# Performance work log

Measured on AMD Instinct MI355X. Metric: run time of the kernel, lower is better.

Reference implementation:

```python
import jax, jax.numpy as jnp
import numpy as np

B, L, DIN = 32, 512, 768
H, DH = 16, 48
DOUT = H * DH
NEG = 1e12


def setup_inputs() -> dict:
    key = jax.random.key(0)
    ks = jax.random.split(key, 8)
    lim = float(np.sqrt(6.0 / (DIN + DOUT)))  # xavier_uniform
    return {
        "Q_seq": jax.random.normal(ks[0], (B, L, DIN), jnp.float32),
        "K_seq": jax.random.normal(ks[1], (B, L, DIN), jnp.float32),
        "V_seq": jax.random.normal(ks[2], (B, L, DIN), jnp.float32),
        "WQ": jax.random.uniform(ks[3], (DIN, DOUT), jnp.float32, -lim, lim),
        "WK": jax.random.uniform(ks[4], (DIN, DOUT), jnp.float32, -lim, lim),
        "WV": jax.random.uniform(ks[5], (DIN, DOUT), jnp.float32, -lim, lim),
        "Q_len": jax.random.randint(ks[6], (B, 1), 0, L, jnp.int64),
        "V_len": jax.random.randint(ks[7], (B, 1), 0, L, jnp.int64),
    }


def reference(Q_seq, K_seq, V_seq, WQ, WK, WV, Q_len, V_len):
    b, l = Q_seq.shape[0], Q_seq.shape[1]
    # projections -> [B, H, L, DH]
    q = (Q_seq @ WQ).reshape(b, l, H, DH).transpose(0, 2, 1, 3)
    k = (K_seq @ WK).reshape(b, l, H, DH).transpose(0, 2, 1, 3)
    v = (V_seq @ WV).reshape(b, l, H, DH).transpose(0, 2, 1, 3)
    # scaled scores [B, H, Lq, Lk]
    A = jnp.einsum("bhqd,bhkd->bhqk", q, k) / jnp.sqrt(jnp.float32(DH))
    # key-length additive mask (original: scatter+cumsum == arange < len)
    mask_k = (jnp.arange(l) < V_len[:, 0][:, None]).astype(A.dtype)  # [B, Lk]
    A = A - (1.0 - mask_k)[:, None, None, :] * NEG
    # causal mask (mask_right=True): subtract on strictly upper triangle
    A = A - jnp.triu(jnp.ones((l, l), A.dtype), 1) * NEG
    A = jax.nn.softmax(A, axis=-1)
    # original quirk: O = A^T @ V  -> O[b,h,k,d] = sum_q A[b,h,q,k] V[b,h,q,d]
    O = jnp.einsum("bhqk,bhqd->bkhd", A, v).reshape(b, l, DOUT)
    # query-length multiplicative mask on output
    mask_q = (jnp.arange(l) < Q_len[:, 0][:, None]).astype(O.dtype)  # [B, L]
    return O * mask_q[:, :, None]
```

## Files before the change

kernel.cpp:

```cpp
#include <hip/hip_runtime.h>
#include <stdint.h>

#define B_    32
#define L_    512
#define DIN_  768
#define H_    16
#define DH_   48
#define DOUT_ 768
#define NHEADS (B_ * H_)
#define HEADELEMS (L_ * DH_)
#define MROWS (B_ * L_)

typedef short bf16x8 __attribute__((ext_vector_type(8)));
typedef float f32x4  __attribute__((ext_vector_type(4)));

__device__ __forceinline__ uint16_t f2bf(float f) {
  uint32_t u = __float_as_uint(f);
  u += 0x7fffu + ((u >> 16) & 1u);
  return (uint16_t)(u >> 16);
}
__device__ __forceinline__ uint32_t pack2bf(float lo, float hi) {
  uint32_t a = __float_as_uint(lo);
  a += 0x7fffu + ((a >> 16) & 1u);
  uint32_t b = __float_as_uint(hi);
  b += 0x7fffu + ((b >> 16) & 1u);
  return (a >> 16) | (b & 0xffff0000u);
}
__device__ __forceinline__ void gload_lds16(const void* g, void* l) {
  __builtin_amdgcn_global_load_lds(
      (const __attribute__((address_space(1))) uint32_t*)g,
      (__attribute__((address_space(3))) uint32_t*)l, 16, 0, 0);
}
__device__ __forceinline__ bf16x8 lds_frag8(const uint16_t* p) {
  union { uint2 u[2]; bf16x8 v; } x;
  x.u[0] = *(const uint2*)(p);
  x.u[1] = *(const uint2*)(p + 4);
  return x.v;
}

__global__ void lens_kernel(const int* __restrict__ qlen_raw,
                            const int* __restrict__ vlen_raw,
                            int* __restrict__ lens) {
  __shared__ int is64[2];
  int t = threadIdx.x;
  if (t < 2) {
    const int* src = (t == 0) ? qlen_raw : vlen_raw;
    int o = 0;
    for (int i = 0; i < 16; ++i) o |= src[2 * i + 1];
    is64[t] = (o == 0) ? 1 : 0;
  }
  __syncthreads();
  int which = t >> 5;
  int i = t & 31;
  const int* src = which ? vlen_raw : qlen_raw;
  lens[t] = is64[which] ? src[2 * i] : src[i];
}

__global__ void wconv_kernel(const float* __restrict__ WQ,
                             const float* __restrict__ WK,
                             const float* __restrict__ WV,
                             uint16_t* __restrict__ Wt) {
  const int z = blockIdx.z;
  const float* W = (z == 0) ? WQ : (z == 1) ? WK : WV;
  const float sc = (z == 0) ? 0.14433756729740643f : 1.0f;
  uint16_t* dst = Wt + (size_t)z * DIN_ * DOUT_;
  const int n  = blockIdx.x * 256 + threadIdx.x;
  const int k4 = blockIdx.y * 4;
  float f0 = W[(size_t)(k4 + 0) * DOUT_ + n] * sc;
  float f1 = W[(size_t)(k4 + 1) * DOUT_ + n] * sc;
  float f2 = W[(size_t)(k4 + 2) * DOUT_ + n] * sc;
  float f3 = W[(size_t)(k4 + 3) * DOUT_ + n] * sc;
  uint2 p;
  p.x = pack2bf(f0, f1);
  p.y = pack2bf(f2, f3);
  *(uint2*)&dst[(size_t)n * DIN_ + k4] = p;
}

__global__ __launch_bounds__(512, 4) void mfma_proj(
    const float* __restrict__ Xq, const float* __restrict__ Xk,
    const float* __restrict__ Xv, const uint16_t* __restrict__ Wt,
    uint16_t* __restrict__ qh, uint16_t* __restrict__ kh,
    uint16_t* __restrict__ vh) {
  const int z = blockIdx.z;
  const float* X = (z == 0) ? Xq : (z == 1) ? Xk : Xv;
  uint16_t* dst  = (z == 0) ? qh : (z == 1) ? kh : vh;
  const uint16_t* W = Wt + (size_t)z * DIN_ * DOUT_;

  __shared__ uint16_t As[2][128][32];
  __shared__ uint16_t Bs[2][256][32];

  const int t  = threadIdx.x;
  const int m0 = blockIdx.x * 128;
  const int n0 = blockIdx.y * 256;

  const int csw = (t & 3) ^ ((t >> 3) & 3);

  const float* aptr = X + (size_t)(m0 + (t >> 2)) * DIN_ + csw * 8;
  char* aWb = (char*)&As[0][0][0] + (t >> 2) * 64 + (t & 3) * 16;

  const uint16_t* bptr0 = W + (size_t)(n0 + (t >> 2)) * DIN_ + csw * 8;
  const uint16_t* bptr1 = W + (size_t)(n0 + 128 + (t >> 2)) * DIN_ + csw * 8;
  char* bB = (char*)&Bs[0][0][0] + t * 16;

  const int w = t >> 6, lane = t & 63;
  const int wm = (w & 1) * 64, wn = (w >> 1) * 64;
  const int fr = lane & 15;
  const int quad = lane >> 4;

  f32x4 acc[4][4];
#pragma unroll
  for (int i = 0; i < 4; ++i)
#pragma unroll
    for (int j = 0; j < 4; ++j) acc[i][j] = f32x4{0.f, 0.f, 0.f, 0.f};

  {
    gload_lds16(bptr0, bB);
    gload_lds16(bptr1, bB + 8192);
    float4 x0 = *(const float4*)(aptr);
    float4 x1 = *(const float4*)(aptr + 4);
    uint4 pA;
    pA.x = pack2bf(x0.x, x0.y); pA.y = pack2bf(x0.z, x0.w);
    pA.z = pack2bf(x1.x, x1.y); pA.w = pack2bf(x1.z, x1.w);
    *(uint4*)aWb = pA;
    __syncthreads();
  }

  int cur = 0;
  for (int kt = 0; kt < DIN_ / 32; ++kt) {
    const int nxt = cur ^ 1;
    float4 x0{}, x1{};
    const bool pre = (kt + 1 < DIN_ / 32);
    if (pre) {
      const int k0 = (kt + 1) * 32;
      gload_lds16(bptr0 + k0, bB + nxt * 16384);
      gload_lds16(bptr1 + k0, bB + nxt * 16384 + 8192);
      x0 = *(const float4*)(aptr + k0);
      x1 = *(const float4*)(aptr + k0 + 4);
    }

    bf16x8 af[4], bfr[4];
#pragma unroll
    for (int i = 0; i < 4; ++i) {
      const int r = wm + i * 16 + fr;
      af[i]  = *(const bf16x8*)&As[cur][r][(quad ^ ((r >> 1) & 3)) * 8];
    }
#pragma unroll
    for (int j = 0; j < 4; ++j) {
      const int r = wn + j * 16 + fr;
      bfr[j] = *(const bf16x8*)&Bs[cur][r][(quad ^ ((r >> 1) & 3)) * 8];
    }
#pragma unroll
    for (int mt = 0; mt < 4; ++mt)
#pragma unroll
      for (int nt = 0; nt < 4; ++nt)
        acc[mt][nt] = __builtin_amdgcn_mfma_f32_16x16x32_bf16(
            af[mt], bfr[nt], acc[mt][nt], 0, 0, 0);

    if (pre) {
      uint4 pA;
      pA.x = pack2bf(x0.x, x0.y); pA.y = pack2bf(x0.z, x0.w);
      pA.z = pack2bf(x1.x, x1.y); pA.w = pack2bf(x1.z, x1.w);
      *(uint4*)(aWb + nxt * 8192) = pA;
    }
    __syncthreads();
    cur = nxt;
  }

#pragma unroll
  for (int mt = 0; mt < 4; ++mt) {
#pragma unroll
    for (int r = 0; r < 4; ++r) {
      const int m  = m0 + wm + mt * 16 + quad * 4 + r;
      const int bb = m >> 9;
      const int l  = m & 511;
#pragma unroll
      for (int nt = 0; nt < 4; ++nt) {
        const int n = n0 + wn + nt * 16 + fr;
        const int h = n / DH_;
        const int d = n - h * DH_;
        dst[(((size_t)bb * H_ + h) * L_ + l) * DH_ + d] = f2bf(acc[mt][nt][r]);
      }
    }
  }
}

__global__ __launch_bounds__(256, 2) void attn_mfma(
    const uint16_t* __restrict__ qh, const uint16_t* __restrict__ kh,
    const uint16_t* __restrict__ vh, const int* __restrict__ lens,
    float* __restrict__ out) {
  const int bh = blockIdx.x;
  const int b  = bh >> 4;
  const int h  = bh & 15;
  const int t    = threadIdx.x;
  const int w    = t >> 6;
  const int lane = t & 63;
  const int l15  = lane & 15;
  const int quad = lane >> 4;

  const int qlen = lens[b];
  const int vlen = lens[32 + b];
  const bool deg = (vlen == 0);
  const size_t head = (size_t)bh * HEADELEMS;

  __shared__ uint16_t Pt[4][128][36];
  __shared__ uint16_t Vt[48][36];
  __shared__ float    prt[4][32];

  const uint16_t* qbase = qh + head;
  const uint16_t* kbase = kh + head;
  const uint16_t* vbase = vh + head;

  f32x4 Oacc[8][3];
#pragma unroll
  for (int i = 0; i < 8; ++i)
#pragma unroll
    for (int dt = 0; dt < 3; ++dt) Oacc[i][dt] = f32x4{0.f, 0.f, 0.f, 0.f};

  for (int g = 0; g < 16; ++g) {
    const int q0 = g * 32;
    const int lim = q0 + 31 - 16 * w;

    __syncthreads();

    if (t < 192) {
      const int vq = t & 31, oct = t >> 5;
      uint4 u = *(const uint4*)(vbase + (size_t)(q0 + vq) * DH_ + oct * 8);
      const int d0 = oct * 8;
      Vt[d0 + 0][vq] = (uint16_t)(u.x);
      Vt[d0 + 1][vq] = (uint16_t)(u.x >> 16);
      Vt[d0 + 2][vq] = (uint16_t)(u.y);
      Vt[d0 + 3][vq] = (uint16_t)(u.y >> 16);
      Vt[d0 + 4][vq] = (uint16_t)(u.z);
      Vt[d0 + 5][vq] = (uint16_t)(u.z >> 16);
      Vt[d0 + 6][vq] = (uint16_t)(u.w);
      Vt[d0 + 7][vq] = (uint16_t)(u.w >> 16);
    }

    bf16x8 aq[2][2];
#pragma unroll
    for (int mt = 0; mt < 2; ++mt) {
      const uint16_t* qp = qbase + (size_t)(q0 + mt * 16 + l15) * DH_;
      aq[mt][0] = *(const bf16x8*)(qp + quad * 8);
      bf16x8 zz = {0, 0, 0, 0, 0, 0, 0, 0};
      aq[mt][1] = zz;
      if (quad < 2) aq[mt][1] = *(const bf16x8*)(qp + 32 + quad * 8);
    }

    float lrun[2][4];
#pragma unroll
    for (int mt = 0; mt < 2; ++mt)
#pragma unroll
      for (int r = 0; r < 4; ++r) lrun[mt][r] = 0.0f;

#pragma unroll
    for (int i = 0; i < 8; ++i) {
      if (64 * i > lim) continue;
      const int kb = 64 * i + 16 * w;
      f32x4 s0 = {0.f, 0.f, 0.f, 0.f};
      f32x4 s1 = {0.f, 0.f, 0.f, 0.f};
      if (!deg) {
        const uint16_t* kp = kbase + (size_t)(kb + l15) * DH_;
        bf16x8 bk0 = *(const bf16x8*)(kp + quad * 8);
        bf16x8 bk1 = {0, 0, 0, 0, 0, 0, 0, 0};
        if (quad < 2) bk1 = *(const bf16x8*)(kp + 32 + quad * 8);
        s0 = __builtin_amdgcn_mfma_f32_16x16x32_bf16(aq[0][0], bk0, s0, 0, 0, 0);
        s0 = __builtin_amdgcn_mfma_f32_16x16x32_bf16(aq[0][1], bk1, s0, 0, 0, 0);
        s1 = __builtin_amdgcn_mfma_f32_16x16x32_bf16(aq[1][0], bk0, s1, 0, 0, 0);
        s1 = __builtin_amdgcn_mfma_f32_16x16x32_bf16(aq[1][1], bk1, s1, 0, 0, 0);
      }
      const int kc  = kb + l15;
      const int row = i * 16 + l15;
#pragma unroll
      for (int mt = 0; mt < 2; ++mt) {
        f32x4 sv = (mt == 0) ? s0 : s1;
        float p4[4];
#pragma unroll
        for (int r = 0; r < 4; ++r) {
          const int qrow = q0 + mt * 16 + quad * 4 + r;
          float e;
          if (deg) {
            e = (kc <= qrow) ? 1.0f : 0.0f;
          } else {
            e = (kc < vlen && kc <= qrow) ? __expf(sv[r]) : 0.0f;
          }
          lrun[mt][r] += e;
          p4[r] = e;
        }
        const int col = mt * 16 + quad * 4;
        *(uint32_t*)&Pt[w][row][col]     = pack2bf(p4[0], p4[1]);
        *(uint32_t*)&Pt[w][row][col + 2] = pack2bf(p4[2], p4[3]);
      }
    }

#pragma unroll
    for (int mt = 0; mt < 2; ++mt)
#pragma unroll
      for (int r = 0; r < 4; ++r) {
        float l = lrun[mt][r];
#pragma unroll
        for (int off = 1; off < 16; off <<= 1) l += __shfl_xor(l, off, 64);
        lrun[mt][r] = l;
      }
    if (l15 == 0) {
#pragma unroll
      for (int mt = 0; mt < 2; ++mt)
#pragma unroll
        for (int r = 0; r < 4; ++r)
          prt[w][mt * 16 + quad * 4 + r] = lrun[mt][r];
    }
    __syncthreads();

    {
      const int q = t & 31;
      const float inv = __builtin_amdgcn_rcpf(
          prt[0][q] + prt[1][q] + prt[2][q] + prt[3][q]);
#pragma unroll
      for (int j = 0; j < 6; ++j) {
        const int d = (t >> 5) + 8 * j;
        float f = __uint_as_float((uint32_t)Vt[d][q] << 16) * inv;
        Vt[d][q] = f2bf(f);
      }
    }
    __syncthreads();

    bf16x8 bv[3];
#pragma unroll
    for (int dt = 0; dt < 3; ++dt)
      bv[dt] = lds_frag8(&Vt[dt * 16 + l15][quad * 8]);
#pragma unroll
    for (int i = 0; i < 8; ++i) {
      if (64 * i > lim) continue;
      bf16x8 ap = lds_frag8(&Pt[w][i * 16 + l15][quad * 8]);
#pragma unroll
      for (int dt = 0; dt < 3; ++dt)
        Oacc[i][dt] = __builtin_amdgcn_mfma_f32_16x16x32_bf16(
            ap, bv[dt], Oacc[i][dt], 0, 0, 0);
    }
  }

#pragma unroll
  for (int i = 0; i < 8; ++i) {
#pragma unroll
    for (int r = 0; r < 4; ++r) {
      const int k_abs = 64 * i + 16 * w + quad * 4 + r;
      const float msk = (k_abs < qlen) ? 1.0f : 0.0f;
      float* orow = out + (size_t)(b * L_ + k_abs) * DOUT_ + h * DH_;
#pragma unroll
      for (int dt = 0; dt < 3; ++dt)
        orow[dt * 16 + l15] = Oacc[i][dt][r] * msk;
    }
  }
}

extern "C" void kernel_launch(void* const* d_in, const int* in_sizes, int n_in,
                              void* d_out, int out_size, void* d_ws, size_t ws_size,
                              hipStream_t stream) {
  const float* Qs  = (const float*)d_in[0];
  const float* Kse = (const float*)d_in[1];
  const float* Vs  = (const float*)d_in[2];
  const float* WQ  = (const float*)d_in[3];
  const float* WK  = (const float*)d_in[4];
  const float* WV  = (const float*)d_in[5];
  const int*   Qlen = (const int*)d_in[6];
  const int*   Vlen = (const int*)d_in[7];
  float* out = (float*)d_out;

  char* ws = (char*)d_ws;
  int* lens = (int*)ws;
  uint16_t* qh  = (uint16_t*)(ws + 256);
  uint16_t* kh  = qh + (size_t)B_ * H_ * L_ * DH_;
  uint16_t* vh  = kh + (size_t)B_ * H_ * L_ * DH_;
  uint16_t* Wt  = vh + (size_t)B_ * H_ * L_ * DH_;

  lens_kernel<<<1, 64, 0, stream>>>(Qlen, Vlen, lens);
  wconv_kernel<<<dim3(3, 192, 3), 256, 0, stream>>>(WQ, WK, WV, Wt);
  mfma_proj<<<dim3(MROWS / 128, DOUT_ / 256, 3), 512, 0, stream>>>(
      Qs, Kse, Vs, Wt, qh, kh, vh);
  attn_mfma<<<NHEADS, 256, 0, stream>>>(qh, kh, vh, lens, out);
}
```

Before: 331.7 us.

## Triple-buffer weight tiles in projection GEMM with explicit vmcnt waits

After: 335.4 us. No clear change (+1.1%).

```diff
diff --git a/kernel.cpp b/kernel.cpp
--- a/kernel.cpp
+++ b/kernel.cpp
@@ -87,11 +87,12 @@
   const uint16_t* W = Wt + (size_t)z * DIN_ * DOUT_;
 
   __shared__ uint16_t As[2][128][32];
-  __shared__ uint16_t Bs[2][256][32];
+  __shared__ uint16_t Bs[3][256][32];
 
   const int t  = threadIdx.x;
   const int m0 = blockIdx.x * 128;
   const int n0 = blockIdx.y * 256;
+  const int NKT = DIN_ / 32;
 
   const int csw = (t & 3) ^ ((t >> 3) & 3);
 
@@ -113,41 +114,47 @@
 #pragma unroll
     for (int j = 0; j < 4; ++j) acc[i][j] = f32x4{0.f, 0.f, 0.f, 0.f};
 
-  {
-    gload_lds16(bptr0, bB);
-    gload_lds16(bptr1, bB + 8192);
-    float4 x0 = *(const float4*)(aptr);
-    float4 x1 = *(const float4*)(aptr + 4);
-    uint4 pA;
-    pA.x = pack2bf(x0.x, x0.y); pA.y = pack2bf(x0.z, x0.w);
-    pA.z = pack2bf(x1.x, x1.y); pA.w = pack2bf(x1.z, x1.w);
-    *(uint4*)aWb = pA;
-    __syncthreads();
-  }
-
-  int cur = 0;
-  for (int kt = 0; kt < DIN_ / 32; ++kt) {
-    const int nxt = cur ^ 1;
-    float4 x0{}, x1{};
-    const bool pre = (kt + 1 < DIN_ / 32);
-    if (pre) {
-      const int k0 = (kt + 1) * 32;
-      gload_lds16(bptr0 + k0, bB + nxt * 16384);
-      gload_lds16(bptr1 + k0, bB + nxt * 16384 + 8192);
-      x0 = *(const float4*)(aptr + k0);
-      x1 = *(const float4*)(aptr + k0 + 4);
-    }
+  float4 x0, x1;
+
+#define STAGE_(j_)                                          \
+  {                                                         \
+    const int k0_ = (j_) * 32;                              \
+    x0 = *(const float4*)(aptr + k0_);                      \
+    x1 = *(const float4*)(aptr + k0_ + 4);                  \
+    gload_lds16(bptr0 + k0_, bB + ((j_) % 3) * 16384);      \
+    gload_lds16(bptr1 + k0_, bB + ((j_) % 3) * 16384 + 8192); \
+  }
+#define PACKA_(j_)                                          \
+  {                                                         \
+    uint4 pA_;                                              \
+    pA_.x = pack2bf(x0.x, x0.y); pA_.y = pack2bf(x0.z, x0.w); \
+    pA_.z = pack2bf(x1.x, x1.y); pA_.w = pack2bf(x1.z, x1.w); \
+    *(uint4*)(aWb + ((j_) % 2) * 8192) = pA_;               \
+  }
+
+  STAGE_(0);
+  PACKA_(0);
+  STAGE_(1);
+  asm volatile("s_waitcnt vmcnt(4) lgkmcnt(0)" ::: "memory");
+  __builtin_amdgcn_s_barrier();
+  __builtin_amdgcn_sched_barrier(0);
+
+  for (int kt = 0; kt < NKT; ++kt) {
+    if (kt + 1 < NKT) PACKA_(kt + 1);
+    if (kt + 2 < NKT) STAGE_(kt + 2);
 
     bf16x8 af[4], bfr[4];
+    const uint16_t(*Acur)[32] = As[kt & 1];
+    const uint16_t(*Bcur)[32] = Bs[kt % 3];
 #pragma unroll
     for (int i = 0; i < 4; ++i) {
       const int r = wm + i * 16 + fr;
-      af[i]  = *(const bf16x8*)&As[cur][r][(quad ^ ((r >> 1) & 3)) * 8];
+      af[i]  = *(const bf16x8*)&Acur[r][(quad ^ ((r >> 1) & 3)) * 8];
     }
 #pragma unroll
     for (int j = 0; j < 4; ++j) {
       const int r = wn + j * 16 + fr;
-      bfr[j] = *(const bf16x8*)&Bs[cur][r][(quad ^ ((r >> 1) & 3)) * 8];
+      bfr[j] = *(const bf16x8*)&Bcur[r][(quad ^ ((r >> 1) & 3)) * 8];
     }
 #pragma unroll
     for (int mt = 0; mt < 4; ++mt)
@@ -156,15 +163,16 @@
         acc[mt][nt] = __builtin_amdgcn_mfma_f32_16x16x32_bf16(
             af[mt], bfr[nt], acc[mt][nt], 0, 0, 0);
 
-    if (pre) {
-      uint4 pA;
-      pA.x = pack2bf(x0.x, x0.y); pA.y = pack2bf(x0.z, x0.w);
-      pA.z = pack2bf(x1.x, x1.y); pA.w = pack2bf(x1.z, x1.w);
-      *(uint4*)(aWb + nxt * 8192) = pA;
-    }
-    __syncthreads();
-    cur = nxt;
-  }
+    if (kt + 2 < NKT) {
+      asm volatile("s_waitcnt vmcnt(4) lgkmcnt(0)" ::: "memory");
+    } else {
+      asm volatile("s_waitcnt vmcnt(0) lgkmcnt(0)" ::: "memory");
+    }
+    __builtin_amdgcn_s_barrier();
+    __builtin_amdgcn_sched_barrier(0);
+  }
+#undef STAGE_
+#undef PACKA_
 
 #pragma unroll
   for (int mt = 0; mt < 4; ++mt) {
```
